# Performance work log

Hardware: AMD Instinct MI355X
Metric: run time of the kernel (lower is better)

Reference implementation:

```python
import jax, jax.numpy as jnp
import numpy as np

B, N, K, H, C = 32, 1000, 10, 128, 2  # K = nb_neighbors + 1 = kernel_size


def setup_inputs() -> dict:
    key = jax.random.key(0)
    ks = jax.random.split(key, 9)
    s = 1.0 / np.sqrt(C * K)
    return {
        "x": jax.random.uniform(ks[0], (B, N, C), dtype=jnp.float32),
        "Wx": jax.random.uniform(ks[1], (H, C, K), jnp.float32, -s, s),  # conv_x weight
        "bx": jax.random.uniform(ks[2], (H,), jnp.float32, -s, s),
        "Wy": jax.random.uniform(ks[3], (H, C, K), jnp.float32, -s, s),  # conv_y weight
        "by": jax.random.uniform(ks[4], (H,), jnp.float32, -s, s),
        "W1": jax.random.normal(ks[5], (C, H), jnp.float32) * 0.5,
        "b1": jnp.zeros((H,), jnp.float32),
        "W2": jax.random.normal(ks[6], (H, H), jnp.float32) * (1.0 / np.sqrt(H)),
        "b2": jnp.zeros((H,), jnp.float32),
    }


def reference(x, Wx, bx, Wy, by, W1, b1, W2, b2):
    # node embedding: (B,N,H)
    node_emb = jnp.einsum("bnc,ch->bnh", x, W1) + b1

    # knn: squared distances give the same ordering as cdist; take K nearest (incl. self)
    d2 = jnp.sum((x[:, :, None, :] - x[:, None, :, :]) ** 2, axis=-1)  # (B,N,N)
    _, idx = jax.lax.top_k(-jax.lax.stop_gradient(d2), K)  # (B,N,K)

    # gather neighbor coords: (B,N,K,2)
    b_ix = jnp.arange(B)[:, None, None]
    coords = x[b_ix, idx]

    # sort neighbors by x-coordinate / y-coordinate along K
    ordx = jnp.argsort(coords[..., 0], axis=-1)
    ordy = jnp.argsort(coords[..., 1], axis=-1)
    sorted_x = jnp.take_along_axis(coords, ordx[..., None], axis=2)  # (B,N,K,2)
    sorted_y = jnp.take_along_axis(coords, ordy[..., None], axis=2)

    # conv1d with kernel covering the full K window -> single output position,
    # equivalent to a full contraction over (channel, position)
    emb_x = jnp.einsum("bnkc,hck->bnh", sorted_x, Wx) + bx
    emb_y = jnp.einsum("bnkc,hck->bnh", sorted_y, Wy) + by
    conv_emb = emb_x + emb_y

    conv_emb = jnp.einsum("bnh,hg->bng", conv_emb, W2) + b2
    return node_emb + conv_emb
```

## Files before the change

### kernel.cpp

```cpp
#include <hip/hip_runtime.h>
#include <cfloat>

#define B_ 32
#define N_ 1000
#define K_ 10
#define H_ 128
#define C_ 2
#define NFEAT 43
#define QPB 32
#define TPQ 8
#define G_ 16
#define CW (1.0f / 16.0f)
#define RING0 2

#define WS_MEFF   0
#define WS_SPK    22016
#define WS_CSTART 534016
#define WS_NEED   566912

typedef float v2f __attribute__((ext_vector_type(2)));

#if defined(__has_builtin)
#if __has_builtin(__builtin_elementwise_fma)
#define HAVE_EW_FMA 1
#endif
#endif

__device__ __forceinline__ void meff_row(
    int r, int g, const float* __restrict__ Wx, const float* __restrict__ bx,
    const float* __restrict__ Wy, const float* __restrict__ by,
    const float* __restrict__ W1, const float* __restrict__ b1,
    const float* __restrict__ W2, const float* __restrict__ b2,
    float* __restrict__ M) {
  float acc = 0.f;
  if (r < 40) {
    const int rp = (r < 20) ? r : r - 20;
    const float* W = (r < 20) ? Wx : Wy;
    const int k = rp >> 1;
    const int c = rp & 1;
    const float* Wcol = W + c * K_ + k;
    for (int h = 0; h < H_; ++h)
      acc = fmaf(Wcol[h * C_ * K_], W2[h * H_ + g], acc);
  } else if (r < 42) {
    acc = W1[(r - 40) * H_ + g];
  } else {
    for (int h = 0; h < H_; ++h)
      acc = fmaf(bx[h] + by[h], W2[h * H_ + g], acc);
    acc += b1[g] + b2[g];
  }
  M[r * H_ + g] = acc;
}

__global__ __launch_bounds__(H_) void build_meff(
    const float* __restrict__ Wx, const float* __restrict__ bx,
    const float* __restrict__ Wy, const float* __restrict__ by,
    const float* __restrict__ W1, const float* __restrict__ b1,
    const float* __restrict__ W2, const float* __restrict__ b2,
    float* __restrict__ M) {
  meff_row(blockIdx.x, threadIdx.x, Wx, bx, Wy, by, W1, b1, W2, b2, M);
}

__global__ __launch_bounds__(256) void prep(
    const float* __restrict__ x,
    const float* __restrict__ Wx, const float* __restrict__ bx,
    const float* __restrict__ Wy, const float* __restrict__ by,
    const float* __restrict__ W1, const float* __restrict__ b1,
    const float* __restrict__ W2, const float* __restrict__ b2,
    float* __restrict__ Meff, float4* __restrict__ spk_g,
    int* __restrict__ cstart_g) {
  const int tid = threadIdx.x;
  if (blockIdx.x >= B_) {
    const int r = blockIdx.x - B_;
    if (tid < H_) meff_row(r, tid, Wx, bx, Wy, by, W1, b1, W2, b2, Meff);
    return;
  }
  const int b = blockIdx.x;
  __shared__ float2 p[N_];
  __shared__ short  cidv[N_];
  __shared__ int    hist[G_ * G_], cur[G_ * G_];

  const float2* xb = (const float2*)(x + (size_t)b * N_ * C_);
  hist[tid] = 0;
  __syncthreads();
  for (int i = tid; i < N_; i += 256) {
    float2 v = xb[i];
    p[i] = v;
    int cxx = min(G_ - 1, max(0, (int)(v.x * (float)G_)));
    int cyy = min(G_ - 1, max(0, (int)(v.y * (float)G_)));
    int c = cyy * G_ + cxx;
    cidv[i] = (short)c;
    atomicAdd(&hist[c], 1);
  }
  __syncthreads();

  if (tid < 64) {
    const int l = tid;
    const int h0 = hist[4 * l], h1 = hist[4 * l + 1];
    const int h2 = hist[4 * l + 2], h3 = hist[4 * l + 3];
    const int T = h0 + h1 + h2 + h3;
    int v = T;
#pragma unroll
    for (int off = 1; off < 64; off <<= 1) {
      const int u = __shfl_up(v, off, 64);
      v += (l >= off) ? u : 0;
    }
    const int E = v - T;
    const int e0 = E, e1 = E + h0, e2 = E + h0 + h1, e3 = E + h0 + h1 + h2;
    cur[4 * l] = e0; cur[4 * l + 1] = e1; cur[4 * l + 2] = e2; cur[4 * l + 3] = e3;
    int* cs = cstart_g + b * (G_ * G_ + 1);
    cs[4 * l] = e0; cs[4 * l + 1] = e1; cs[4 * l + 2] = e2; cs[4 * l + 3] = e3;
    if (l == 63) cs[G_ * G_] = N_;
  }
  __syncthreads();

  for (int i = tid; i < N_; i += 256) {
    int c = cidv[i];
    int pos = atomicAdd(&cur[c], 1);
    spk_g[b * N_ + pos] =
        make_float4(p[i].x, p[i].y, __int_as_float((i << 16) | pos), 0.f);
  }
}

__device__ __forceinline__ unsigned long long shflx64(unsigned long long v, int msk) {
  const unsigned lo = __shfl_xor((unsigned)(v & 0xffffffffull), msk, 64);
  const unsigned hi = __shfl_xor((unsigned)(v >> 32), msk, 64);
  return ((unsigned long long)hi << 32) | lo;
}

#define INSERT_LDS(j)                                                          \
  {                                                                            \
    const float4 pk = spk[(j)];                                                \
    const float dx = __fsub_rn(px, pk.x);                                      \
    const float dy = __fsub_rn(py, pk.y);                                      \
    const float dd = __fadd_rn(__fmul_rn(dx, dx), __fmul_rn(dy, dy));          \
    const unsigned long long key =                                             \
        ((unsigned long long)__float_as_uint(dd) << 32) |                      \
        (unsigned)__float_as_int(pk.z);                                        \
    bool c[K_];                                                                \
    _Pragma("unroll") for (int kk = 0; kk < K_; ++kk) c[kk] = key < bk[kk];    \
    _Pragma("unroll") for (int kk = K_ - 1; kk >= 1; --kk)                     \
        bk[kk] = c[kk - 1] ? bk[kk - 1] : (c[kk] ? key : bk[kk]);              \
    bk[0] = c[0] ? key : bk[0];                                                \
  }

#define MERGE_GATHER(tenth_out)                                                \
  {                                                                            \
    _Pragma("unroll") for (int s2 = 0; s2 < K_; ++s2) {                        \
      unsigned long long m = bk[0];                                            \
      unsigned long long o = shflx64(m, 1); m = (o < m) ? o : m;               \
      o = shflx64(m, 2); m = (o < m) ? o : m;                                  \
      o = shflx64(m, 4); m = (o < m) ? o : m;                                  \
      const bool pop = (bk[0] == m);                                           \
      _Pragma("unroll") for (int k2 = 0; k2 < K_ - 1; ++k2)                    \
          bk[k2] = pop ? bk[k2 + 1] : bk[k2];                                  \
      bk[K_ - 1] = pop ? ~0ull : bk[K_ - 1];                                   \
      const int spos = min((int)(m & 0xffffull), N_ - 1);                      \
      const float4 c4 = spk[spos];                                             \
      feat[2 * s2]          = c4.x;                                            \
      feat[2 * s2 + 1]      = c4.y;                                            \
      feat[20 + 2 * s2]     = c4.x;                                            \
      feat[20 + 2 * s2 + 1] = c4.y;                                            \
      if (s2 == K_ - 1) (tenth_out) = m;                                       \
    }                                                                          \
  }

__global__ __launch_bounds__(QPB * TPQ, 4) void conv_knn(
    const float4* __restrict__ spk_g, const int* __restrict__ cstart_g,
    const float* __restrict__ Meff, float* __restrict__ out) {
  __shared__ __align__(16) float4 spk[N_];
  __shared__ int    cstart[G_ * G_ + 1];
  __shared__ __align__(16) float smem[NFEAT * H_];

  const int b = blockIdx.y, tid = threadIdx.x;
  const int q = tid >> 3, t = tid & 7;
  const int s = blockIdx.x * QPB + q;
  const bool valid = (s < N_);

  const float4* spg = spk_g + (size_t)b * N_;
  for (int i = tid; i < N_; i += QPB * TPQ) spk[i] = spg[i];
  for (int i = tid; i < G_ * G_ + 1; i += QPB * TPQ)
    cstart[i] = cstart_g[b * (G_ * G_ + 1) + i];
  __syncthreads();

  float px = 0.f, py = 0.f;
  int cx = 0, cy = 0;
  if (valid) {
    px = spk[s].x; py = spk[s].y;
    cx = min(G_ - 1, max(0, (int)(px * (float)G_)));
    cy = min(G_ - 1, max(0, (int)(py * (float)G_)));
  }

  unsigned long long bk[K_];
#pragma unroll
  for (int k = 0; k < K_; ++k) bk[k] = ~0ull;

  const int X0 = max(cx - RING0, 0), X1 = min(cx + RING0, G_ - 1);
  const int Y0 = max(cy - RING0, 0), Y1 = min(cy + RING0, G_ - 1);
  if (valid) {
    for (int yy = Y0; yy <= Y1; ++yy) {
      const int s0 = cstart[yy * G_ + X0];
      const int s1 = cstart[yy * G_ + X1 + 1];
      for (int j = s0 + t; j < s1; j += TPQ) INSERT_LDS(j);
    }
  }

  float feat[NFEAT];
  unsigned long long tenth = ~0ull;
  MERGE_GATHER(tenth);

  bool done = true;
  if (valid) {
    const bool have10 = (tenth != ~0ull);
    const float tau = __uint_as_float((unsigned)(tenth >> 32));
    float R = 1e30f;
    if (X0 > 0)      R = fminf(R, px - (float)X0 * CW);
    if (X1 < G_ - 1) R = fminf(R, (float)(X1 + 1) * CW - px);
    if (Y0 > 0)      R = fminf(R, py - (float)Y0 * CW);
    if (Y1 < G_ - 1) R = fminf(R, (float)(Y1 + 1) * CW - py);
    const bool fullg = (X0 == 0) && (X1 == G_ - 1) && (Y0 == 0) && (Y1 == G_ - 1);
    const float Rs = R - 1e-6f;
    done = fullg || (have10 && Rs > 0.f && tau < Rs * Rs);
  }

  if (__syncthreads_and(done ? 1 : 0) == 0) {
    const bool redo = valid && !done;
    if (redo) {
#pragma unroll
      for (int k = 0; k < K_; ++k) bk[k] = ~0ull;
      for (int j = t; j < N_; j += TPQ) INSERT_LDS(j);
    }
    if (redo) {
      unsigned long long tenth2;
      MERGE_GATHER(tenth2);
    }
  }

  for (int i = tid; i < NFEAT * H_; i += QPB * TPQ) smem[i] = Meff[i];

  if (valid) {
#pragma unroll
    for (int p = 0; p < K_ - 1; ++p) {
#pragma unroll
      for (int u = 0; u < K_ - 1 - p; ++u) {
        const bool sw = feat[2 * u + 2] < feat[2 * u];
        const float ax = feat[2 * u], ay = feat[2 * u + 1];
        feat[2 * u]     = sw ? feat[2 * u + 2] : ax;
        feat[2 * u + 1] = sw ? feat[2 * u + 3] : ay;
        feat[2 * u + 2] = sw ? ax : feat[2 * u + 2];
        feat[2 * u + 3] = sw ? ay : feat[2 * u + 3];
      }
    }
#pragma unroll
    for (int p = 0; p < K_ - 1; ++p) {
#pragma unroll
      for (int u = 0; u < K_ - 1 - p; ++u) {
        const int e = 20 + 2 * u;
        const bool sw = feat[e + 3] < feat[e + 1];
        const float ax = feat[e], ay = feat[e + 1];
        feat[e]     = sw ? feat[e + 2] : ax;
        feat[e + 1] = sw ? feat[e + 3] : ay;
        feat[e + 2] = sw ? ax : feat[e + 2];
        feat[e + 3] = sw ? ay : feat[e + 3];
      }
    }
    feat[40] = px;
    feat[41] = py;
    feat[42] = 1.f;
  }
  __syncthreads();

  if (valid) {
    const int otar = __float_as_int(spk[s].z) >> 16;
    float* op = out + ((size_t)(b * N_ + otar)) * H_;
    const float4* M4 = (const float4*)smem;
#pragma unroll
    for (int j = 0; j < 4; ++j) {
      v2f a0 = {0.f, 0.f}, a1 = {0.f, 0.f};
#pragma unroll
      for (int r = 0; r < NFEAT; ++r) {
        const float4 m = M4[r * 32 + j * 8 + t];
        const float f = feat[r];
#ifdef HAVE_EW_FMA
        const v2f ff = {f, f};
        const v2f m0 = {m.x, m.y};
        const v2f m1 = {m.z, m.w};
        a0 = __builtin_elementwise_fma(ff, m0, a0);
        a1 = __builtin_elementwise_fma(ff, m1, a1);
#else
        a0.x = fmaf(f, m.x, a0.x);
        a0.y = fmaf(f, m.y, a0.y);
        a1.x = fmaf(f, m.z, a1.x);
        a1.y = fmaf(f, m.w, a1.y);
#endif
      }
      *(float4*)&op[j * 32 + 4 * t] = make_float4(a0.x, a0.y, a1.x, a1.y);
    }
  }
}
#undef INSERT_LDS
#undef MERGE_GATHER

#define LSTRIDE 170
__global__ __launch_bounds__(256, 4) void conv_emb_fb(
    const float* __restrict__ x, const float* __restrict__ Meff,
    float* __restrict__ out) {
  __shared__ float2 pts[N_];
  __shared__ float  smem[NFEAT * H_];
  __shared__ int    midx[32 * K_];

  const int b   = blockIdx.y;
  const int tid = threadIdx.x;
  const int q   = tid >> 3;
  const int t   = tid & 7;
  const int n   = blockIdx.x * 32 + q;
  const bool valid = (n < N_);

  const float2* xb = (const float2*)(x + (size_t)b * N_ * C_);
  for (int i = tid; i < N_; i += 256) pts[i] = xb[i];
  __syncthreads();

  float px = 0.f, py = 0.f;
  if (valid) { px = pts[n].x; py = pts[n].y; }

  float bd[K_]; int bi[K_];
#pragma unroll
  for (int k = 0; k < K_; ++k) { bd[k] = FLT_MAX; bi[k] = 0; }

#pragma unroll 2
  for (int m = 0; m < N_ / 8; ++m) {
    const int j = t + m * 8;
    const float2 p = pts[j];
    const float dx = __fsub_rn(px, p.x);
    const float dy = __fsub_rn(py, p.y);
    const float d  = __fadd_rn(__fmul_rn(dx, dx), __fmul_rn(dy, dy));
    bool c[K_];
#pragma unroll
    for (int s = 0; s < K_; ++s) c[s] = d < bd[s];
#pragma unroll
    for (int s = K_ - 1; s >= 1; --s) {
      bd[s] = c[s - 1] ? bd[s - 1] : (c[s] ? d : bd[s]);
      bi[s] = c[s - 1] ? bi[s - 1] : (c[s] ? j : bi[s]);
    }
    bd[0] = c[0] ? d : bd[0];
    bi[0] = c[0] ? j : bi[0];
  }

  const int lbase = q * LSTRIDE + t * 2 * K_;
#pragma unroll
  for (int e = 0; e < K_; ++e) {
    smem[lbase + 2 * e]     = bd[e];
    smem[lbase + 2 * e + 1] = __int_as_float(bi[e]);
  }
  __syncthreads();

  if (t == 0 && valid) {
    int cc[8];
#pragma unroll
    for (int tt = 0; tt < 8; ++tt) cc[tt] = 0;
    const int mb = q * LSTRIDE;
#pragma unroll
    for (int s = 0; s < K_; ++s) {
      float bdv = FLT_MAX; int biv = 0x7fffffff; int bt = 0;
#pragma unroll
      for (int tt = 0; tt < 8; ++tt) {
        const int off = mb + tt * 2 * K_ + cc[tt] * 2;
        const float hd = smem[off];
        const int   hi = __float_as_int(smem[off + 1]);
        const bool take = (hd < bdv) || ((hd == bdv) && (hi < biv));
        bdv = take ? hd : bdv;
        biv = take ? hi : biv;
        bt  = take ? tt : bt;
      }
      midx[q * K_ + s] = biv;
#pragma unroll
      for (int tt = 0; tt < 8; ++tt) cc[tt] += (bt == tt) ? 1 : 0;
    }
  }
  __syncthreads();

  int ridx[K_];
  if (valid) {
#pragma unroll
    for (int k = 0; k < K_; ++k) ridx[k] = midx[q * K_ + k];
  }
  for (int i = tid; i < NFEAT * H_; i += 256) smem[i] = Meff[i];

  float feat[NFEAT];
  if (valid) {
#pragma unroll
    for (int k = 0; k < K_; ++k) {
      const float2 c = pts[ridx[k]];
      feat[2 * k]          = c.x;
      feat[2 * k + 1]      = c.y;
      feat[20 + 2 * k]     = c.x;
      feat[20 + 2 * k + 1] = c.y;
    }
#pragma unroll
    for (int p = 0; p < K_ - 1; ++p) {
#pragma unroll
      for (int u = 0; u < K_ - 1 - p; ++u) {
        const bool sw = feat[2 * u + 2] < feat[2 * u];
        const float ax = feat[2 * u], ay = feat[2 * u + 1];
        feat[2 * u]     = sw ? feat[2 * u + 2] : ax;
        feat[2 * u + 1] = sw ? feat[2 * u + 3] : ay;
        feat[2 * u + 2] = sw ? ax : feat[2 * u + 2];
        feat[2 * u + 3] = sw ? ay : feat[2 * u + 3];
      }
    }
#pragma unroll
    for (int p = 0; p < K_ - 1; ++p) {
#pragma unroll
      for (int u = 0; u < K_ - 1 - p; ++u) {
        const int e = 20 + 2 * u;
        const bool sw = feat[e + 3] < feat[e + 1];
        const float ax = feat[e], ay = feat[e + 1];
        feat[e]     = sw ? feat[e + 2] : ax;
        feat[e + 1] = sw ? feat[e + 3] : ay;
        feat[e + 2] = sw ? ax : feat[e + 2];
        feat[e + 3] = sw ? ay : feat[e + 3];
      }
    }
    feat[40] = px;
    feat[41] = py;
    feat[42] = 1.f;
  }
  __syncthreads();

  if (valid) {
    float* op = out + ((size_t)(b * N_ + n)) * H_;
#pragma unroll 2
    for (int gi = 0; gi < H_ / 8; ++gi) {
      const int g = gi * 8 + t;
      float acc = 0.f;
#pragma unroll
      for (int r = 0; r < NFEAT; ++r)
        acc = fmaf(feat[r], smem[r * H_ + g], acc);
      op[g] = acc;
    }
  }
}

extern "C" void kernel_launch(void* const* d_in, const int* in_sizes, int n_in,
                              void* d_out, int out_size, void* d_ws, size_t ws_size,
                              hipStream_t stream) {
  const float* x  = (const float*)d_in[0];
  const float* Wx = (const float*)d_in[1];
  const float* bx = (const float*)d_in[2];
  const float* Wy = (const float*)d_in[3];
  const float* by = (const float*)d_in[4];
  const float* W1 = (const float*)d_in[5];
  const float* b1 = (const float*)d_in[6];
  const float* W2 = (const float*)d_in[7];
  const float* b2 = (const float*)d_in[8];
  float* o = (float*)d_out;

  char* ws = (char*)d_ws;
  float*  Meff     = (float*)(ws + WS_MEFF);
  float4* spk_g    = (float4*)(ws + WS_SPK);
  int*    cstart_g = (int*)(ws + WS_CSTART);

  if (ws_size >= (size_t)WS_NEED) {
    prep<<<dim3(B_ + NFEAT), dim3(256), 0, stream>>>(
        x, Wx, bx, Wy, by, W1, b1, W2, b2, Meff, spk_g, cstart_g);
    conv_knn<<<dim3((N_ + QPB - 1) / QPB, B_), dim3(QPB * TPQ), 0, stream>>>(
        spk_g, cstart_g, Meff, o);
  } else {
    build_meff<<<dim3(NFEAT), dim3(H_), 0, stream>>>(Wx, bx, Wy, by, W1, b1, W2, b2, Meff);
    conv_emb_fb<<<dim3((N_ + 31) / 32, B_), dim3(256), 0, stream>>>(x, Meff, o);
  }
}
```

Before: 32.55 us.

## Fuse per-batch grid binning into conv_knn and drop the global spk workspace

The separate prep kernel that binned points into a 16x16 grid and wrote sorted points and cell starts to global memory is removed. Each conv_knn block now rebuilds the histogram, prefix scan and bucketed point list in shared memory straight from x, reusing the smem weight buffer as scratch. Meff is built by its own small kernel. This removes a global round trip and the dependency on prep, but every block (32 per batch) now redoes the binning work, and a kernel launch is still needed for Meff.

```diff
diff --git a/kernel.cpp b/kernel.cpp
--- a/kernel.cpp
+++ b/kernel.cpp
@@ -14,9 +14,7 @@
 #define RING0 2
 
 #define WS_MEFF   0
-#define WS_SPK    22016
-#define WS_CSTART 534016
-#define WS_NEED   566912
+#define WS_NEED   22016
 
 typedef float v2f __attribute__((ext_vector_type(2)));
 
@@ -26,12 +24,14 @@
 #endif
 #endif
 
-__device__ __forceinline__ void meff_row(
-    int r, int g, const float* __restrict__ Wx, const float* __restrict__ bx,
+__global__ __launch_bounds__(H_) void build_meff(
+    const float* __restrict__ Wx, const float* __restrict__ bx,
     const float* __restrict__ Wy, const float* __restrict__ by,
     const float* __restrict__ W1, const float* __restrict__ b1,
     const float* __restrict__ W2, const float* __restrict__ b2,
     float* __restrict__ M) {
+  const int r = blockIdx.x;
+  const int g = threadIdx.x;
   float acc = 0.f;
   if (r < 40) {
     const int rp = (r < 20) ? r : r - 20;
@@ -49,76 +49,6 @@
     acc += b1[g] + b2[g];
   }
   M[r * H_ + g] = acc;
-}
-
-__global__ __launch_bounds__(H_) void build_meff(
-    const float* __restrict__ Wx, const float* __restrict__ bx,
-    const float* __restrict__ Wy, const float* __restrict__ by,
-    const float* __restrict__ W1, const float* __restrict__ b1,
-    const float* __restrict__ W2, const float* __restrict__ b2,
-    float* __restrict__ M) {
-  meff_row(blockIdx.x, threadIdx.x, Wx, bx, Wy, by, W1, b1, W2, b2, M);
-}
-
-__global__ __launch_bounds__(256) void prep(
-    const float* __restrict__ x,
-    const float* __restrict__ Wx, const float* __restrict__ bx,
-    const float* __restrict__ Wy, const float* __restrict__ by,
-    const float* __restrict__ W1, const float* __restrict__ b1,
-    const float* __restrict__ W2, const float* __restrict__ b2,
-    float* __restrict__ Meff, float4* __restrict__ spk_g,
-    int* __restrict__ cstart_g) {
-  const int tid = threadIdx.x;
-  if (blockIdx.x >= B_) {
-    const int r = blockIdx.x - B_;
-    if (tid < H_) meff_row(r, tid, Wx, bx, Wy, by, W1, b1, W2, b2, Meff);
-    return;
-  }
-  const int b = blockIdx.x;
-  __shared__ float2 p[N_];
-  __shared__ short  cidv[N_];
-  __shared__ int    hist[G_ * G_], cur[G_ * G_];
-
-  const float2* xb = (const float2*)(x + (size_t)b * N_ * C_);
-  hist[tid] = 0;
-  __syncthreads();
-  for (int i = tid; i < N_; i += 256) {
-    float2 v = xb[i];
-    p[i] = v;
-    int cxx = min(G_ - 1, max(0, (int)(v.x * (float)G_)));
-    int cyy = min(G_ - 1, max(0, (int)(v.y * (float)G_)));
-    int c = cyy * G_ + cxx;
-    cidv[i] = (short)c;
-    atomicAdd(&hist[c], 1);
-  }
-  __syncthreads();
-
-  if (tid < 64) {
-    const int l = tid;
-    const int h0 = hist[4 * l], h1 = hist[4 * l + 1];
-    const int h2 = hist[4 * l + 2], h3 = hist[4 * l + 3];
-    const int T = h0 + h1 + h2 + h3;
-    int v = T;
-#pragma unroll
-    for (int off = 1; off < 64; off <<= 1) {
-      const int u = __shfl_up(v, off, 64);
-      v += (l >= off) ? u : 0;
-    }
-    const int E = v - T;
-    const int e0 = E, e1 = E + h0, e2 = E + h0 + h1, e3 = E + h0 + h1 + h2;
-    cur[4 * l] = e0; cur[4 * l + 1] = e1; cur[4 * l + 2] = e2; cur[4 * l + 3] = e3;
-    int* cs = cstart_g + b * (G_ * G_ + 1);
-    cs[4 * l] = e0; cs[4 * l + 1] = e1; cs[4 * l + 2] = e2; cs[4 * l + 3] = e3;
-    if (l == 63) cs[G_ * G_] = N_;
-  }
-  __syncthreads();
-
-  for (int i = tid; i < N_; i += 256) {
-    int c = cidv[i];
-    int pos = atomicAdd(&cur[c], 1);
-    spk_g[b * N_ + pos] =
-        make_float4(p[i].x, p[i].y, __int_as_float((i << 16) | pos), 0.f);
-  }
 }
 
 __device__ __forceinline__ unsigned long long shflx64(unsigned long long v, int msk) {
@@ -165,27 +95,83 @@
   }
 
 __global__ __launch_bounds__(QPB * TPQ, 4) void conv_knn(
-    const float4* __restrict__ spk_g, const int* __restrict__ cstart_g,
-    const float* __restrict__ Meff, float* __restrict__ out) {
+    const float* __restrict__ x, const float* __restrict__ Meff,
+    float* __restrict__ out) {
   __shared__ __align__(16) float4 spk[N_];
   __shared__ int    cstart[G_ * G_ + 1];
   __shared__ __align__(16) float smem[NFEAT * H_];
+  int* hist = (int*)smem;
+  int* cur  = ((int*)smem) + 256;
 
   const int b = blockIdx.y, tid = threadIdx.x;
   const int q = tid >> 3, t = tid & 7;
-  const int s = blockIdx.x * QPB + q;
-  const bool valid = (s < N_);
-
-  const float4* spg = spk_g + (size_t)b * N_;
-  for (int i = tid; i < N_; i += QPB * TPQ) spk[i] = spg[i];
-  for (int i = tid; i < G_ * G_ + 1; i += QPB * TPQ)
-    cstart[i] = cstart_g[b * (G_ * G_ + 1) + i];
+  const int n = blockIdx.x * QPB + q;
+  const bool valid = (n < N_);
+
+  const float2* xb = (const float2*)(x + (size_t)b * N_ * C_);
+
+  float2 sp[4];
+  int    sc[4];
+#pragma unroll
+  for (int k = 0; k < 4; ++k) {
+    const int i = tid + k * 256;
+    if (i < N_) {
+      const float2 v = xb[i];
+      sp[k] = v;
+      const int cxx = min(G_ - 1, max(0, (int)(v.x * (float)G_)));
+      const int cyy = min(G_ - 1, max(0, (int)(v.y * (float)G_)));
+      sc[k] = cyy * G_ + cxx;
+    } else {
+      sc[k] = -1;
+    }
+  }
+  hist[tid] = 0;
+  __syncthreads();
+#pragma unroll
+  for (int k = 0; k < 4; ++k)
+    if (sc[k] >= 0) atomicAdd(&hist[sc[k]], 1);
+  __syncthreads();
+
+  if (tid < 64) {
+    const int l = tid;
+    const int h0 = hist[4 * l], h1 = hist[4 * l + 1];
+    const int h2 = hist[4 * l + 2], h3 = hist[4 * l + 3];
+    const int T = h0 + h1 + h2 + h3;
+    int v = T;
+#pragma unroll
+    for (int off = 1; off < 64; off <<= 1) {
+      const int u = __shfl_up(v, off, 64);
+      v += (l >= off) ? u : 0;
+    }
+    const int E = v - T;
+    cur[4 * l] = E;
+    cur[4 * l + 1] = E + h0;
+    cur[4 * l + 2] = E + h0 + h1;
+    cur[4 * l + 3] = E + h0 + h1 + h2;
+    cstart[4 * l] = E;
+    cstart[4 * l + 1] = E + h0;
+    cstart[4 * l + 2] = E + h0 + h1;
+    cstart[4 * l + 3] = E + h0 + h1 + h2;
+    if (l == 63) cstart[G_ * G_] = N_;
+  }
+  __syncthreads();
+
+#pragma unroll
+  for (int k = 0; k < 4; ++k) {
+    if (sc[k] >= 0) {
+      const int i = tid + k * 256;
+      const int pos = atomicAdd(&cur[sc[k]], 1);
+      spk[pos] = make_float4(sp[k].x, sp[k].y,
+                             __int_as_float((i << 16) | pos), 0.f);
+    }
+  }
   __syncthreads();
 
   float px = 0.f, py = 0.f;
   int cx = 0, cy = 0;
   if (valid) {
-    px = spk[s].x; py = spk[s].y;
+    const float2 v = xb[n];
+    px = v.x; py = v.y;
     cx = min(G_ - 1, max(0, (int)(px * (float)G_)));
     cy = min(G_ - 1, max(0, (int)(py * (float)G_)));
   }
@@ -235,6 +221,7 @@
     }
   }
 
+  __syncthreads();
   for (int i = tid; i < NFEAT * H_; i += QPB * TPQ) smem[i] = Meff[i];
 
   if (valid) {
@@ -270,8 +257,7 @@
   __syncthreads();
 
   if (valid) {
-    const int otar = __float_as_int(spk[s].z) >> 16;
-    float* op = out + ((size_t)(b * N_ + otar)) * H_;
+    float* op = out + ((size_t)(b * N_ + n)) * H_;
     const float4* M4 = (const float4*)smem;
 #pragma unroll
     for (int j = 0; j < 4; ++j) {
@@ -446,8 +432,8 @@
   const float* x  = (const float*)d_in[0];
   const float* Wx = (const float*)d_in[1];
   const float* bx = (const float*)d_in[2];
+  const float* by_ = (const float*)d_in[4];
   const float* Wy = (const float*)d_in[3];
-  const float* by = (const float*)d_in[4];
   const float* W1 = (const float*)d_in[5];
   const float* b1 = (const float*)d_in[6];
   const float* W2 = (const float*)d_in[7];
@@ -455,17 +441,13 @@
   float* o = (float*)d_out;
 
   char* ws = (char*)d_ws;
-  float*  Meff     = (float*)(ws + WS_MEFF);
-  float4* spk_g    = (float4*)(ws + WS_SPK);
-  int*    cstart_g = (int*)(ws + WS_CSTART);
+  float* Meff = (float*)(ws + WS_MEFF);
+
+  build_meff<<<dim3(NFEAT), dim3(H_), 0, stream>>>(Wx, bx, Wy, by_, W1, b1, W2, b2, Meff);
 
   if (ws_size >= (size_t)WS_NEED) {
-    prep<<<dim3(B_ + NFEAT), dim3(256), 0, stream>>>(
-        x, Wx, bx, Wy, by, W1, b1, W2, b2, Meff, spk_g, cstart_g);
-    conv_knn<<<dim3((N_ + QPB - 1) / QPB, B_), dim3(QPB * TPQ), 0, stream>>>(
-        spk_g, cstart_g, Meff, o);
+    conv_knn<<<dim3((N_ + QPB - 1) / QPB, B_), dim3(QPB * TPQ), 0, stream>>>(x, Meff, o);
   } else {
-    build_meff<<<dim3(NFEAT), dim3(H_), 0, stream>>>(Wx, bx, Wy, by, W1, b1, W2, b2, Meff);
     conv_emb_fb<<<dim3((N_ + 31) / 32, B_), dim3(256), 0, stream>>>(x, Meff, o);
   }
 }
```

Result: slower. 34.22 us (+5.1%).
